# Performance work log

Hardware: AMD Instinct MI355X
Metric: run time of the kernel (lower is better)

The kernel has to match this reference:

```python
import jax, jax.numpy as jnp
import numpy as np

B, T, D_IN, H, BR, D_OUT = 256, 500, 700, 200, 2, 35
V_TH = 1.0


def setup_inputs() -> dict:
    key = jax.random.key(0)
    ks = jax.random.split(key, 7)
    x = jax.random.normal(ks[0], (B, T, D_IN), dtype=jnp.float32)
    W_in = jax.random.normal(ks[1], (H * BR, D_IN), dtype=jnp.float32) * (1.0 / np.sqrt(D_IN))
    b_in = jax.random.normal(ks[2], (H * BR,), dtype=jnp.float32) * 0.01
    # tau_n ~ U(0, 4) per branch per neuron (as in SimpleDH_LIF init)
    tau_n = jax.random.uniform(ks[3], (H, BR), dtype=jnp.float32, minval=0.0, maxval=4.0)
    tau_m = jnp.full((H,), 2.0, dtype=jnp.float32)  # torch init: tensor(2.0) per neuron
    W_out = jax.random.normal(ks[5], (D_OUT, H), dtype=jnp.float32) * (1.0 / np.sqrt(H))
    b_out = jax.random.normal(ks[6], (D_OUT,), dtype=jnp.float32) * 0.01
    return {"x": x, "W_in": W_in, "b_in": b_in, "tau_n": tau_n,
            "tau_m": tau_m, "W_out": W_out, "b_out": b_out}


def reference(x, W_in, b_in, tau_n, tau_m, W_out, b_out):
    b, t, _ = x.shape
    # Batched input projection for all timesteps at once: (B,T,H*BR) -> (T,B,H,BR)
    branch_in = jnp.einsum('bti,oi->bto', x, W_in) + b_in
    branch_in = branch_in.reshape(b, t, H, BR).transpose(1, 0, 2, 3)

    beta = jax.nn.sigmoid(tau_n)          # (H, BR) dendritic branch decay
    alpha = jax.nn.sigmoid(tau_m)         # (H,)   soma membrane decay

    def step(carry, inp_t):
        v, i_d, counts = carry            # v:(B,H) i_d:(B,H,BR) counts:(B,H)
        i_d = beta * i_d + (1.0 - beta) * inp_t
        i_total = i_d.sum(axis=-1)        # (B,H)
        v = alpha * v + (1.0 - alpha) * i_total
        spike = (v >= V_TH).astype(v.dtype)
        v = v - spike * V_TH
        return (v, i_d, counts + spike), None

    v0 = jnp.zeros((b, H), dtype=x.dtype)
    i0 = jnp.zeros((b, H, BR), dtype=x.dtype)
    c0 = jnp.zeros((b, H), dtype=x.dtype)
    (v, i_d, spike_counts), _ = jax.lax.scan(step, (v0, i0, c0), branch_in)

    return spike_counts @ W_out.T + b_out  # (B, D_OUT)
```

## Files before the change

### kernel.cpp

```cpp
#include <hip/hip_runtime.h>

#define B_   256
#define T_   500
#define DIN  700
#define KP   704
#define H_   200
#define NO   400
#define DOUT 35
#define NKC  22

typedef _Float16 half_t;
typedef __attribute__((ext_vector_type(8))) _Float16 half8;
typedef __attribute__((ext_vector_type(4))) float floatx4;

#define SX 16.0f
#define SW 4096.0f
#define INV_S (1.0f / 65536.0f)

__device__ __forceinline__ float sigmoidf_(float x) {
    return 1.0f / (1.0f + expf(-x));
}

__global__ __launch_bounds__(256) void cvt_wfrag(
    const float* __restrict__ W, half_t* __restrict__ Whf, half_t* __restrict__ Wlf)
{
    int t = blockIdx.x * 256 + threadIdx.x;
    if (t >= NKC * 25 * 64) return;
    int lane = t & 63;
    int rest = t >> 6;
    int nfg  = rest % 25;
    int kc   = rest / 25;
    int la = lane & 15, lb = lane >> 4;
    int row = nfg * 16 + la;
    int col = kc * 32 + lb * 8;
    half8 hh, ll;
    #pragma unroll
    for (int j = 0; j < 8; ++j) {
        float v = (col + j < DIN) ? W[(size_t)row * DIN + col + j] : 0.0f;
        float s = v * SW;
        half_t h = (half_t)s;
        hh[j] = h;
        ll[j] = (half_t)(s - (float)h);
    }
    *reinterpret_cast<half8*>(&Whf[(size_t)t * 8]) = hh;
    *reinterpret_cast<half8*>(&Wlf[(size_t)t * 8]) = ll;
}

__global__ __launch_bounds__(256, 3) void dh_gemm_w32(
    const float* __restrict__ x,
    const half_t* __restrict__ Whf, const half_t* __restrict__ Wlf,
    const float* __restrict__ bin, float* __restrict__ Y)
{
    int p = blockIdx.x;
    int L = (p & 7) * 625 + (p >> 3);
    int by = L / 5, bx = L - by * 5;

    const int w    = threadIdx.x >> 6;
    const int lane = threadIdx.x & 63;
    const int la   = lane & 15;
    const int lb   = lane >> 4;

    const int m0 = by * 128 + w * 32;
    const int o0 = bx * 80;

    floatx4 acc[2][5];
    #pragma unroll
    for (int mf = 0; mf < 2; ++mf)
        #pragma unroll
        for (int nf = 0; nf < 5; ++nf) {
            floatx4 z = {0.f, 0.f, 0.f, 0.f};
            acc[mf][nf] = z;
        }

    size_t arow[2];
    #pragma unroll
    for (int mf = 0; mf < 2; ++mf)
        arow[mf] = (size_t)(m0 + mf * 16 + la) * DIN;
    const size_t bbase = ((size_t)(bx * 5) * 64 + lane) * 8;

    float4 raA[2][2], raB[2][2];

    auto LOADA = [&](float4 (&ra)[2][2], int kc) {
        const int col = kc * 32 + lb * 8;
        const int c2ofs = (col + 8 <= DIN) ? 4 : (692 - col);
        #pragma unroll
        for (int mf = 0; mf < 2; ++mf) {
            const float* ptr = &x[arow[mf] + col];
            ra[mf][0] = *reinterpret_cast<const float4*>(ptr);
            ra[mf][1] = *reinterpret_cast<const float4*>(ptr + c2ofs);
        }
    };

    auto COMPUTE = [&](const float4 (&ra)[2][2], int kc) {
        half8 bh[5], bl[5];
        const size_t kofs = (size_t)kc * 25 * 64 * 8;
        #pragma unroll
        for (int nf = 0; nf < 5; ++nf) {
            size_t idx = bbase + kofs + (size_t)nf * 64 * 8;
            bh[nf] = *reinterpret_cast<const half8*>(&Whf[idx]);
            bl[nf] = *reinterpret_cast<const half8*>(&Wlf[idx]);
        }
        half8 ah[2], al[2];
        #pragma unroll
        for (int mf = 0; mf < 2; ++mf) {
            float vv[8];
            *reinterpret_cast<float4*>(&vv[0]) = ra[mf][0];
            *reinterpret_cast<float4*>(&vv[4]) = ra[mf][1];
            half8 hh, ll;
            #pragma unroll
            for (int j = 0; j < 8; ++j) {
                float s = vv[j] * SX;
                half_t h = (half_t)s;
                hh[j] = h;
                ll[j] = (half_t)(s - (float)h);
            }
            ah[mf] = hh;
            al[mf] = ll;
        }
        #pragma unroll
        for (int mf = 0; mf < 2; ++mf)
            #pragma unroll
            for (int nf = 0; nf < 5; ++nf)
                acc[mf][nf] = __builtin_amdgcn_mfma_f32_16x16x32_f16(ah[mf], bh[nf], acc[mf][nf], 0, 0, 0);
        #pragma unroll
        for (int mf = 0; mf < 2; ++mf)
            #pragma unroll
            for (int nf = 0; nf < 5; ++nf)
                acc[mf][nf] = __builtin_amdgcn_mfma_f32_16x16x32_f16(ah[mf], bl[nf], acc[mf][nf], 0, 0, 0);
        #pragma unroll
        for (int mf = 0; mf < 2; ++mf)
            #pragma unroll
            for (int nf = 0; nf < 5; ++nf)
                acc[mf][nf] = __builtin_amdgcn_mfma_f32_16x16x32_f16(al[mf], bh[nf], acc[mf][nf], 0, 0, 0);
    };

    LOADA(raA, 0);
    #pragma unroll 1
    for (int kc = 0; kc < NKC; kc += 2) {
        LOADA(raB, kc + 1);
        COMPUTE(raA, kc);
        if (kc + 2 < NKC) LOADA(raA, kc + 2);
        COMPUTE(raB, kc + 1);
    }

    float bo[5];
    #pragma unroll
    for (int nf = 0; nf < 5; ++nf) bo[nf] = bin[o0 + nf * 16 + la];

    #pragma unroll
    for (int mf = 0; mf < 2; ++mf) {
        int mbase = m0 + mf * 16 + lb * 4;
        #pragma unroll
        for (int rg = 0; rg < 4; ++rg) {
            int mm = mbase + rg;
            int bb = mm / T_;
            int tt = mm - bb * T_;
            float* yrow = &Y[((size_t)tt * B_ + bb) * NO + o0 + la];
            #pragma unroll
            for (int nf = 0; nf < 5; ++nf)
                yrow[nf * 16] = acc[mf][nf][rg] * INV_S + bo[nf];
        }
    }
}

#define BM 256
#define BN 64
#define BK 16
__global__ __launch_bounds__(256) void dh_gemm_in(
    const float* __restrict__ x, const float* __restrict__ Wt,
    const float* __restrict__ bin, float* __restrict__ Y)
{
    __shared__ float As[BK][BM + 4];
    __shared__ float Bs[BK][BN + 4];
    const int tid = threadIdx.x;
    const int tx = tid & 7;
    const int ty = tid >> 3;
    const int m0 = blockIdx.y * BM;
    const int o0 = blockIdx.x * BN;

    float acc[8][8];
    #pragma unroll
    for (int r = 0; r < 8; ++r)
        #pragma unroll
        for (int c = 0; c < 8; ++c) acc[r][c] = 0.0f;

    const int srow = tid >> 2;
    const int skq  = (tid & 3) << 2;

    for (int k0 = 0; k0 < DIN; k0 += BK) {
        float4 areg[4];
        #pragma unroll
        for (int i = 0; i < 4; ++i) {
            int idx = tid + i * 256;
            int row = idx >> 2;
            int kq  = (idx & 3) << 2;
            int kg  = k0 + kq;
            if (kg < DIN)
                areg[i] = *reinterpret_cast<const float4*>(&x[(size_t)(m0 + row) * DIN + kg]);
            else
                areg[i] = make_float4(0.f, 0.f, 0.f, 0.f);
        }
        float4 breg;
        {
            int kg = k0 + skq;
            int o  = o0 + srow;
            if (kg < DIN && o < NO)
                breg = *reinterpret_cast<const float4*>(&Wt[(size_t)o * DIN + kg]);
            else
                breg = make_float4(0.f, 0.f, 0.f, 0.f);
        }
        __syncthreads();
        #pragma unroll
        for (int i = 0; i < 4; ++i) {
            int idx = tid + i * 256;
            int row = idx >> 2;
            int kq  = (idx & 3) << 2;
            As[kq + 0][row] = areg[i].x;
            As[kq + 1][row] = areg[i].y;
            As[kq + 2][row] = areg[i].z;
            As[kq + 3][row] = areg[i].w;
        }
        Bs[skq + 0][srow] = breg.x;
        Bs[skq + 1][srow] = breg.y;
        Bs[skq + 2][srow] = breg.z;
        Bs[skq + 3][srow] = breg.w;
        __syncthreads();

        #pragma unroll
        for (int k = 0; k < BK; ++k) {
            float a[8], bb[8];
            *reinterpret_cast<float4*>(&a[0])  = *reinterpret_cast<const float4*>(&As[k][ty * 8]);
            *reinterpret_cast<float4*>(&a[4])  = *reinterpret_cast<const float4*>(&As[k][ty * 8 + 4]);
            *reinterpret_cast<float4*>(&bb[0]) = *reinterpret_cast<const float4*>(&Bs[k][tx * 8]);
            *reinterpret_cast<float4*>(&bb[4]) = *reinterpret_cast<const float4*>(&Bs[k][tx * 8 + 4]);
            #pragma unroll
            for (int r = 0; r < 8; ++r)
                #pragma unroll
                for (int c = 0; c < 8; ++c)
                    acc[r][c] = fmaf(a[r], bb[c], acc[r][c]);
        }
    }

    float bo[8];
    #pragma unroll
    for (int c = 0; c < 8; ++c) {
        int o = o0 + tx * 8 + c;
        bo[c] = (o < NO) ? bin[o] : 0.0f;
    }
    const int ob = o0 + tx * 8;
    if (ob < NO) {
        #pragma unroll
        for (int r = 0; r < 8; ++r) {
            int m = m0 + ty * 8 + r;
            int b = m / T_;
            int t = m - b * T_;
            float* yrow = &Y[((size_t)t * B_ + b) * NO];
            float4 v0 = make_float4(acc[r][0] + bo[0], acc[r][1] + bo[1],
                                    acc[r][2] + bo[2], acc[r][3] + bo[3]);
            float4 v1 = make_float4(acc[r][4] + bo[4], acc[r][5] + bo[5],
                                    acc[r][6] + bo[6], acc[r][7] + bo[7]);
            *reinterpret_cast<float4*>(&yrow[ob])     = v0;
            *reinterpret_cast<float4*>(&yrow[ob + 4]) = v1;
        }
    }
}

__global__ __launch_bounds__(64) void dh_scan(
    const float* __restrict__ Y, const float* __restrict__ tau_n,
    const float* __restrict__ tau_m, float* __restrict__ counts)
{
    int g = blockIdx.x * 64 + threadIdx.x;
    int b = g / H_;
    int h = g - b * H_;
    (void)b;
    float beta0 = sigmoidf_(tau_n[h * 2 + 0]);
    float beta1 = sigmoidf_(tau_n[h * 2 + 1]);
    float alpha = sigmoidf_(tau_m[h]);
    float omb0 = 1.0f - beta0, omb1 = 1.0f - beta1, oma = 1.0f - alpha;
    const float2* Yp = reinterpret_cast<const float2*>(Y);

    float v = 0.f, i0 = 0.f, i1 = 0.f, cnt = 0.f;
    #pragma unroll 1
    for (int t0 = 0; t0 < T_; t0 += 10) {
        float2 yb[10];
        #pragma unroll
        for (int j = 0; j < 10; ++j)
            yb[j] = Yp[(size_t)(t0 + j) * (B_ * H_) + g];
        #pragma unroll
        for (int j = 0; j < 10; ++j) {
            i0 = beta0 * i0 + omb0 * yb[j].x;
            i1 = beta1 * i1 + omb1 * yb[j].y;
            float it = i0 + i1;
            v = alpha * v + oma * it;
            if (v >= 1.0f) { v -= 1.0f; cnt += 1.0f; }
        }
    }
    counts[g] = cnt;
}

__global__ __launch_bounds__(64) void dh_out(
    const float* __restrict__ counts, const float* __restrict__ W_out,
    const float* __restrict__ b_out, float* __restrict__ out)
{
    int b = blockIdx.x;
    int o = threadIdx.x;
    if (o >= DOUT) return;
    float acc = b_out[o];
    const float* c = &counts[(size_t)b * H_];
    const float* w = &W_out[(size_t)o * H_];
    #pragma unroll 4
    for (int h = 0; h < H_; ++h)
        acc = fmaf(c[h], w[h], acc);
    out[(size_t)b * DOUT + o] = acc;
}

extern "C" void kernel_launch(void* const* d_in, const int* in_sizes, int n_in,
                              void* d_out, int out_size, void* d_ws, size_t ws_size,
                              hipStream_t stream) {
    const float* x     = (const float*)d_in[0];
    const float* W_in  = (const float*)d_in[1];
    const float* b_in  = (const float*)d_in[2];
    const float* tau_n = (const float*)d_in[3];
    const float* tau_m = (const float*)d_in[4];
    const float* W_out = (const float*)d_in[5];
    const float* b_out = (const float*)d_in[6];
    float* out = (float*)d_out;

    float* Y      = (float*)d_ws;
    float* counts = Y + (size_t)T_ * B_ * NO;

    const size_t nfrag_halves = (size_t)NKC * 25 * 64 * 8;
    size_t need = ((size_t)T_ * B_ * NO + (size_t)B_ * H_) * 4
                + 2 * nfrag_halves * 2;

    if (ws_size >= need) {
        half_t* Whf = (half_t*)(counts + (size_t)B_ * H_);
        half_t* Wlf = Whf + nfrag_halves;

        cvt_wfrag<<<(NKC * 25 * 64 + 255) / 256, 256, 0, stream>>>(W_in, Whf, Wlf);
        dh_gemm_w32<<<5000, 256, 0, stream>>>(x, Whf, Wlf, b_in, Y);
    } else {
        dim3 g1(7, 500);
        dh_gemm_in<<<g1, 256, 0, stream>>>(x, W_in, b_in, Y);
    }

    dh_scan<<<(B_ * H_) / 64, 64, 0, stream>>>(Y, tau_n, tau_m, counts);
    dh_out<<<B_, 64, 0, stream>>>(counts, W_out, b_out, out);
}
```

Baseline: 440.0 us.

## Stage x tiles into LDS via async global_load_lds with triple-buffered pipeline

The GEMM kernel now streams x tiles into a per-wave, XOR-swizzled LDS ring of three buffers using direct global-to-LDS loads. It keeps three sets of W fragments in flight, with explicit vmcnt/lgkmcnt waits, sched barriers and setprio around the MFMA blocks. The goal is to hide global memory latency behind MFMA work and to read A fragments from LDS without bank conflicts. In exchange it lowers launch-bound occupancy to 2 blocks, adds 48KB of LDS per block and more registers, and relies on hand-counted wait values.

```diff
diff --git a/kernel.cpp b/kernel.cpp
--- a/kernel.cpp
+++ b/kernel.cpp
@@ -3,7 +3,6 @@
 #define B_   256
 #define T_   500
 #define DIN  700
-#define KP   704
 #define H_   200
 #define NO   400
 #define DOUT 35
@@ -19,6 +18,13 @@
 
 __device__ __forceinline__ float sigmoidf_(float x) {
     return 1.0f / (1.0f + expf(-x));
+}
+
+__device__ __forceinline__ void gload_lds16(const float* g, float* l) {
+    __builtin_amdgcn_global_load_lds(
+        (const __attribute__((address_space(1))) unsigned int*)g,
+        (__attribute__((address_space(3))) unsigned int*)l,
+        16, 0, 0);
 }
 
 __global__ __launch_bounds__(256) void cvt_wfrag(
@@ -46,11 +52,13 @@
     *reinterpret_cast<half8*>(&Wlf[(size_t)t * 8]) = ll;
 }
 
-__global__ __launch_bounds__(256, 3) void dh_gemm_w32(
+__global__ __launch_bounds__(256, 2) void dh_gemm_3d(
     const float* __restrict__ x,
     const half_t* __restrict__ Whf, const half_t* __restrict__ Wlf,
     const float* __restrict__ bin, float* __restrict__ Y)
 {
+    __shared__ float Abuf[4][3][1024];
+
     int p = blockIdx.x;
     int L = (p & 7) * 625 + (p >> 3);
     int by = L / 5, bx = L - by * 5;
@@ -72,75 +80,157 @@
             acc[mf][nf] = z;
         }
 
-    size_t arow[2];
-    #pragma unroll
-    for (int mf = 0; mf < 2; ++mf)
-        arow[mf] = (size_t)(m0 + mf * 16 + la) * DIN;
-    const size_t bbase = ((size_t)(bx * 5) * 64 + lane) * 8;
-
-    float4 raA[2][2], raB[2][2];
-
-    auto LOADA = [&](float4 (&ra)[2][2], int kc) {
-        const int col = kc * 32 + lb * 8;
-        const int c2ofs = (col + 8 <= DIN) ? 4 : (692 - col);
-        #pragma unroll
-        for (int mf = 0; mf < 2; ++mf) {
-            const float* ptr = &x[arow[mf] + col];
-            ra[mf][0] = *reinterpret_cast<const float4*>(ptr);
-            ra[mf][1] = *reinterpret_cast<const float4*>(ptr + c2ofs);
-        }
-    };
-
-    auto COMPUTE = [&](const float4 (&ra)[2][2], int kc) {
-        half8 bh[5], bl[5];
-        const size_t kofs = (size_t)kc * 25 * 64 * 8;
-        #pragma unroll
-        for (int nf = 0; nf < 5; ++nf) {
-            size_t idx = bbase + kofs + (size_t)nf * 64 * 8;
-            bh[nf] = *reinterpret_cast<const half8*>(&Whf[idx]);
-            bl[nf] = *reinterpret_cast<const half8*>(&Wlf[idx]);
-        }
-        half8 ah[2], al[2];
-        #pragma unroll
-        for (int mf = 0; mf < 2; ++mf) {
-            float vv[8];
-            *reinterpret_cast<float4*>(&vv[0]) = ra[mf][0];
-            *reinterpret_cast<float4*>(&vv[4]) = ra[mf][1];
-            half8 hh, ll;
-            #pragma unroll
-            for (int j = 0; j < 8; ++j) {
-                float s = vv[j] * SX;
-                half_t h = (half_t)s;
-                hh[j] = h;
-                ll[j] = (half_t)(s - (float)h);
-            }
-            ah[mf] = hh;
-            al[mf] = ll;
-        }
-        #pragma unroll
-        for (int mf = 0; mf < 2; ++mf)
-            #pragma unroll
-            for (int nf = 0; nf < 5; ++nf)
-                acc[mf][nf] = __builtin_amdgcn_mfma_f32_16x16x32_f16(ah[mf], bh[nf], acc[mf][nf], 0, 0, 0);
-        #pragma unroll
-        for (int mf = 0; mf < 2; ++mf)
-            #pragma unroll
-            for (int nf = 0; nf < 5; ++nf)
-                acc[mf][nf] = __builtin_amdgcn_mfma_f32_16x16x32_f16(ah[mf], bl[nf], acc[mf][nf], 0, 0, 0);
-        #pragma unroll
-        for (int mf = 0; mf < 2; ++mf)
-            #pragma unroll
-            for (int nf = 0; nf < 5; ++nf)
-                acc[mf][nf] = __builtin_amdgcn_mfma_f32_16x16x32_f16(al[mf], bh[nf], acc[mf][nf], 0, 0, 0);
-    };
-
-    LOADA(raA, 0);
+    const int srow = lane >> 3;
+    const int sseg = (lane & 7) ^ srow;
+    const float* a0 = x + (size_t)(m0 +  0 + srow) * DIN + sseg * 4;
+    const float* a1 = x + (size_t)(m0 +  8 + srow) * DIN + sseg * 4;
+    const float* a2 = x + (size_t)(m0 + 16 + srow) * DIN + sseg * 4;
+    const float* a3 = x + (size_t)(m0 + 24 + srow) * DIN + sseg * 4;
+
+    const half_t* pWh = Whf + ((size_t)(bx * 5) * 64 + lane) * 8;
+    const half_t* pWl = Wlf + ((size_t)(bx * 5) * 64 + lane) * 8;
+
+    const int o00 = (la) * 32      + (((lb * 2)     ^ (la & 7)) << 2);
+    const int o01 = (la) * 32      + (((lb * 2 + 1) ^ (la & 7)) << 2);
+    const int o10 = (16 + la) * 32 + (((lb * 2)     ^ (la & 7)) << 2);
+    const int o11 = (16 + la) * 32 + (((lb * 2 + 1) ^ (la & 7)) << 2);
+
+    half8 B0h[5], B0l[5], B1h[5], B1l[5], B2h[5], B2l[5];
+    half8 ah[2], al[2];
+    float4 f00, f01, f10, f11;
+
+#define STAGE(r) do {                                                   \
+        float* d = &Abuf[w][r][0];                                      \
+        gload_lds16(a0, d);                                             \
+        gload_lds16(a1, d + 256);                                       \
+        gload_lds16(a2, d + 512);                                       \
+        gload_lds16(a3, d + 768);                                       \
+        a0 += 32; a1 += 32; a2 += 32; a3 += 32;                         \
+    } while (0)
+
+#define LOADB(RH, RL) do {                                              \
+        _Pragma("unroll")                                               \
+        for (int nf = 0; nf < 5; ++nf) {                                \
+            RH[nf] = *reinterpret_cast<const half8*>(pWh + nf * 512);   \
+            RL[nf] = *reinterpret_cast<const half8*>(pWl + nf * 512);   \
+        }                                                               \
+        pWh += 12800; pWl += 12800;                                     \
+    } while (0)
+
+#define DSR(r) do {                                                     \
+        const float* bse = &Abuf[w][r][0];                              \
+        f00 = *reinterpret_cast<const float4*>(bse + o00);              \
+        f01 = *reinterpret_cast<const float4*>(bse + o01);              \
+        f10 = *reinterpret_cast<const float4*>(bse + o10);              \
+        f11 = *reinterpret_cast<const float4*>(bse + o11);              \
+    } while (0)
+
+#define CONV() do {                                                     \
+        _Pragma("unroll")                                               \
+        for (int mf = 0; mf < 2; ++mf) {                                \
+            float vv[8];                                                \
+            *reinterpret_cast<float4*>(&vv[0]) = mf ? f10 : f00;        \
+            *reinterpret_cast<float4*>(&vv[4]) = mf ? f11 : f01;        \
+            half8 hh, ll;                                               \
+            _Pragma("unroll")                                           \
+            for (int j = 0; j < 8; ++j) {                               \
+                float s = vv[j] * SX;                                   \
+                half_t h = (half_t)s;                                   \
+                hh[j] = h;                                              \
+                ll[j] = (half_t)(s - (float)h);                         \
+            }                                                           \
+            ah[mf] = hh; al[mf] = ll;                                   \
+        }                                                               \
+    } while (0)
+
+#define MFMAS(RH, RL) do {                                              \
+        _Pragma("unroll")                                               \
+        for (int mf = 0; mf < 2; ++mf)                                  \
+            _Pragma("unroll")                                           \
+            for (int nf = 0; nf < 5; ++nf)                              \
+                acc[mf][nf] = __builtin_amdgcn_mfma_f32_16x16x32_f16(ah[mf], RH[nf], acc[mf][nf], 0, 0, 0); \
+        _Pragma("unroll")                                               \
+        for (int mf = 0; mf < 2; ++mf)                                  \
+            _Pragma("unroll")                                           \
+            for (int nf = 0; nf < 5; ++nf)                              \
+                acc[mf][nf] = __builtin_amdgcn_mfma_f32_16x16x32_f16(ah[mf], RL[nf], acc[mf][nf], 0, 0, 0); \
+        _Pragma("unroll")                                               \
+        for (int mf = 0; mf < 2; ++mf)                                  \
+            _Pragma("unroll")                                           \
+            for (int nf = 0; nf < 5; ++nf)                              \
+                acc[mf][nf] = __builtin_amdgcn_mfma_f32_16x16x32_f16(al[mf], RH[nf], acc[mf][nf], 0, 0, 0); \
+    } while (0)
+
+#define WAITVM(N) asm volatile("s_waitcnt vmcnt(" #N ")" ::: "memory"); __builtin_amdgcn_sched_barrier(0)
+#define WAITLG()  asm volatile("s_waitcnt lgkmcnt(0)" ::: "memory"); __builtin_amdgcn_sched_barrier(0)
+#define SBAR()    __builtin_amdgcn_sched_barrier(0)
+
+#define BODY(r)  do {                                                   \
+        WAITVM(38);                    \
+        DSR(r);                                                         \
+        WAITLG();                 \
+        STAGE(r); SBAR();             \
+        CONV();                                                         \
+        WAITVM(32);                                   \
+        __builtin_amdgcn_s_setprio(1);                                  \
+        MFMAS(B##r##h, B##r##l);                                        \
+        __builtin_amdgcn_s_setprio(0); SBAR();                          \
+        LOADB(B##r##h, B##r##l);             \
+    } while (0)
+
+    STAGE(0); SBAR();
+    LOADB(B0h, B0l); SBAR();
+    STAGE(1); SBAR();
+    LOADB(B1h, B1l); SBAR();
+    STAGE(2); SBAR();
+    LOADB(B2h, B2l); SBAR();
+
     #pragma unroll 1
-    for (int kc = 0; kc < NKC; kc += 2) {
-        LOADA(raB, kc + 1);
-        COMPUTE(raA, kc);
-        if (kc + 2 < NKC) LOADA(raA, kc + 2);
-        COMPUTE(raB, kc + 1);
+    for (int I = 0; I < 6; ++I) {
+        BODY(0);
+        BODY(1);
+        BODY(2);
+    }
+
+    {
+        WAITVM(38);
+        DSR(0);
+        WAITLG();
+        {
+            int colf = 21 * 32 + sseg * 4;
+            colf = (colf > 696) ? 696 : colf;
+            const float* c0 = x + (size_t)(m0 +  0 + srow) * DIN + colf;
+            const float* c1 = x + (size_t)(m0 +  8 + srow) * DIN + colf;
+            const float* c2 = x + (size_t)(m0 + 16 + srow) * DIN + colf;
+            const float* c3 = x + (size_t)(m0 + 24 + srow) * DIN + colf;
+            float* d = &Abuf[w][0][0];
+            gload_lds16(c0, d);
+            gload_lds16(c1, d + 256);
+            gload_lds16(c2, d + 512);
+            gload_lds16(c3, d + 768);
+        }
+        SBAR();
+        CONV();
+        WAITVM(32);
+        __builtin_amdgcn_s_setprio(1);
+        MFMAS(B0h, B0l);
+        __builtin_amdgcn_s_setprio(0); SBAR();
+        LOADB(B0h, B0l);
+    }
+    {
+        WAITVM(38); DSR(1); WAITLG(); CONV();
+        WAITVM(28);
+        __builtin_amdgcn_s_setprio(1); MFMAS(B1h, B1l); __builtin_amdgcn_s_setprio(0); SBAR();
+    }
+    {
+        WAITVM(24); DSR(2); WAITLG(); CONV();
+        WAITVM(14);
+        __builtin_amdgcn_s_setprio(1); MFMAS(B2h, B2l); __builtin_amdgcn_s_setprio(0); SBAR();
+    }
+    {
+        WAITVM(10); DSR(0); WAITLG(); CONV();
+        WAITVM(0);
+        __builtin_amdgcn_s_setprio(1); MFMAS(B0h, B0l); __builtin_amdgcn_s_setprio(0); SBAR();
     }
 
     float bo[5];
@@ -161,6 +251,15 @@
                 yrow[nf * 16] = acc[mf][nf][rg] * INV_S + bo[nf];
         }
     }
+#undef STAGE
+#undef LOADB
+#undef DSR
+#undef CONV
+#undef MFMAS
+#undef WAITVM
+#undef WAITLG
+#undef SBAR
+#undef BODY
 }
 
 #define BM 256
@@ -338,7 +437,7 @@
         half_t* Wlf = Whf + nfrag_halves;
 
         cvt_wfrag<<<(NKC * 25 * 64 + 255) / 256, 256, 0, stream>>>(W_in, Whf, Wlf);
-        dh_gemm_w32<<<5000, 256, 0, stream>>>(x, Whf, Wlf, b_in, Y);
+        dh_gemm_3d<<<5000, 256, 0, stream>>>(x, Whf, Wlf, b_in, Y);
     } else {
         dim3 g1(7, 500);
         dh_gemm_in<<<g1, 256, 0, stream>>>(x, W_in, b_in, Y);
```

After: 426.2 us. 1.03x faster.
